# Kernel optimization log

Measured on AMD Instinct MI355X. Metric: run time of the kernel, lower is better.

Reference implementation:

```python
import jax, jax.numpy as jnp
import numpy as np

D_MODEL = 512
N_HEADS = 8
D_K = D_MODEL // N_HEADS


def setup_inputs() -> dict:
    key = jax.random.key(0)
    ks = jax.random.split(key, 12)
    B, S = 2, 4096
    std = 1.0 / np.sqrt(D_MODEL)
    inp = {
        "q": jax.random.normal(ks[0], (B, S, D_MODEL), jnp.float32),
        "k": jax.random.normal(ks[1], (B, S, D_MODEL), jnp.float32),
        "v": jax.random.normal(ks[2], (B, S, D_MODEL), jnp.float32),
        "Wq": jax.random.normal(ks[3], (D_MODEL, D_MODEL), jnp.float32) * std,
        "bq": jnp.zeros((D_MODEL,), jnp.float32),
        "Wk": jax.random.normal(ks[4], (D_MODEL, D_MODEL), jnp.float32) * std,
        "bk": jnp.zeros((D_MODEL,), jnp.float32),
        "Wv": jax.random.normal(ks[5], (D_MODEL, D_MODEL), jnp.float32) * std,
        "bv": jnp.zeros((D_MODEL,), jnp.float32),
        "Wo": jax.random.normal(ks[6], (D_MODEL, D_MODEL), jnp.float32) * std,
        "bo": jnp.zeros((D_MODEL,), jnp.float32),
        # torch init: ones
        "time_decay": jnp.ones((1, N_HEADS, 1, 1), jnp.float32) * 0.01,
        "scale": jnp.ones((1,), jnp.float32),
    }
    return inp


def reference(q, k, v, Wq, bq, Wk, bk, Wv, bv, Wo, bo, time_decay, scale):
    B, S, _ = q.shape
    # projections (torch Linear: x @ W.T + b), reshape to [B, H, S, d_k]
    def proj(x, W, b):
        y = x @ W.T + b
        return y.reshape(B, -1, N_HEADS, D_K).transpose(0, 2, 1, 3)

    qh = proj(q, Wq, bq)
    kh = proj(k, Wk, bk)
    vh = proj(v, Wv, bv)

    # scores: [B, H, Sq, Sk]
    scores = jnp.einsum("bhqd,bhkd->bhqk", qh, kh) / np.sqrt(D_K)
    scores = scores * scale
    # exponential decay over absolute key position (per-head learnable rate)
    pos = jnp.arange(S, dtype=scores.dtype)  # key positions
    decay = jnp.exp(-time_decay * jnp.abs(pos)[None, None, None, :])  # [1,H,1,Sk]
    scores = scores * decay

    attn = jax.nn.softmax(scores, axis=-1)
    context = jnp.einsum("bhqk,bhkd->bhqd", attn, vh)
    context = context.transpose(0, 2, 1, 3).reshape(B, S, D_MODEL)
    out = context @ Wo.T + bo
    return out
```

## Files before the change

### kernel.cpp

```cpp
#include <hip/hip_runtime.h>
#include <hip/hip_bf16.h>
#include <stdint.h>

typedef __attribute__((ext_vector_type(8))) __bf16 bf16x8;
typedef __attribute__((ext_vector_type(4))) float f32x4;
typedef __attribute__((ext_vector_type(16))) float f32x16;
typedef __attribute__((ext_vector_type(8))) unsigned short ushort8;
typedef __attribute__((ext_vector_type(4))) unsigned short ushort4v;
typedef __attribute__((ext_vector_type(2))) unsigned int uint2v;
typedef __attribute__((ext_vector_type(4))) unsigned int uint4v;

__device__ __forceinline__ unsigned short bfbits(float x) {
    __bf16 b = (__bf16)x;
    return __builtin_bit_cast(unsigned short, b);
}
__device__ __forceinline__ float bf2f_u(unsigned short u) {
    return __builtin_bit_cast(float, (unsigned int)u << 16);
}

__device__ __forceinline__ f32x4 mfma16(bf16x8 a, bf16x8 b, f32x4 c) {
    return __builtin_amdgcn_mfma_f32_16x16x32_bf16(a, b, c, 0, 0, 0);
}
__device__ __forceinline__ f32x16 mfma32(bf16x8 a, bf16x8 b, f32x16 c) {
    return __builtin_amdgcn_mfma_f32_32x32x16_bf16(a, b, c, 0, 0, 0);
}

__device__ __forceinline__ unsigned int cvtpk(float lo, float hi) {
    unsigned int r;
    asm("v_cvt_pk_bf16_f32 %0, %1, %2" : "=v"(r) : "v"(lo), "v"(hi));
    return r;
}

__device__ __forceinline__ float lanepull(float src, int srcl) {
    return __builtin_bit_cast(float,
        __builtin_amdgcn_ds_bpermute(srcl * 4, __builtin_bit_cast(int, src)));
}

__device__ __forceinline__ void gload16(const void* g, void* l) {
    __builtin_amdgcn_global_load_lds(
        (const __attribute__((address_space(1))) unsigned int*)g,
        (__attribute__((address_space(3))) unsigned int*)l, 16, 0, 0);
}

__device__ __forceinline__ f32x16 zero16() {
    f32x16 r;
    #pragma unroll
    for (int i = 0; i < 16; i++) r[i] = 0.f;
    return r;
}

__device__ __forceinline__ int tail_tiles(float tdh, float scale) {
    float cut = 5.3f + __logf(fmaxf(scale, 1e-20f));
    cut = fmaxf(cut, 0.f);
    tdh = fmaxf(tdh, 1e-8f);
    int kt = (int)ceilf(cut / (tdh * 64.f));
    if (kt < 1) kt = 1;
    if (kt > 64) kt = 64;
    return kt;
}

__global__ __launch_bounds__(256) void wconv(
    const float* __restrict__ Wq, const float* __restrict__ Wk,
    const float* __restrict__ Wv, const float* __restrict__ Wo,
    unsigned short* __restrict__ Wbf)
{
    const int t    = blockIdx.x * 256 + threadIdx.x;
    const int slab = t >> 15;
    const int off8 = t & 32767;
    const float* src = (slab == 0) ? Wq : (slab == 1) ? Wk : (slab == 2) ? Wv : Wo;
    float4 a = ((const float4*)(src + off8 * 8))[0];
    float4 b = ((const float4*)(src + off8 * 8))[1];
    uint4v pk = { cvtpk(a.x, a.y), cvtpk(a.z, a.w), cvtpk(b.x, b.y), cvtpk(b.z, b.w) };
    *(uint4v*)(Wbf + (size_t)slab * 262144 + off8 * 8) = pk;
}

__global__ __launch_bounds__(256) void gemm_qkv(
    const float* __restrict__ q, const float* __restrict__ k, const float* __restrict__ v,
    const unsigned short* __restrict__ Wbf,
    const float* __restrict__ bq, const float* __restrict__ bk, const float* __restrict__ bv,
    const float* __restrict__ td, const float* __restrict__ sc,
    unsigned short* __restrict__ Qh, unsigned short* __restrict__ Kh,
    unsigned short* __restrict__ Vt)
{
    __shared__ __align__(16) char ALDS[2][16384];

    const int id  = blockIdx.x;
    const int nid = (id & 7) * 96 + (id >> 3);
    const int z   = nid >> 8;
    const int rem = nid & 255;
    const int bm  = rem >> 2;
    const int bn  = rem & 3;

    const float* A0   = (z == 0) ? q  : (z == 1) ? k  : v;
    const float* bias = (z == 0) ? bq : (z == 1) ? bk : bv;

    const int tid  = threadIdx.x;
    const int lane = tid & 63;
    const int w    = tid >> 6;
    const int wm   = w >> 1, wn = w & 1;
    const int l15  = lane & 15;
    const int g    = lane >> 4;

    const int lr  = lane >> 3;
    const int lc  = ((lane & 7) * 16) ^ (lr << 4);
    const char* asrc[4];
    #pragma unroll
    for (int j = 0; j < 4; j++)
        asrc[j] = (const char*)A0 + (size_t)(bm * 128 + w * 32 + j * 8 + lr) * 2048 + lc;
    int adst[4];
    #pragma unroll
    for (int j = 0; j < 4; j++) adst[j] = w * 4096 + j * 1024;

    const unsigned short* Bp[4];
    #pragma unroll
    for (int n = 0; n < 4; n++)
        Bp[n] = Wbf + (size_t)z * 262144
              + (size_t)(bn * 128 + wn * 64 + n * 16 + l15) * 512 + g * 8;

    f32x4 acc[4][4];
    #pragma unroll
    for (int m = 0; m < 4; m++)
        #pragma unroll
        for (int n = 0; n < 4; n++)
            acc[m][n] = (f32x4){0.f, 0.f, 0.f, 0.f};

    const int arow = l15;
    const int asw  = (arow & 7) << 4;

    #pragma unroll
    for (int j = 0; j < 4; j++) gload16(asrc[j], ALDS[0] + adst[j]);
    bf16x8 BA[4], BB[4];
    #pragma unroll
    for (int n = 0; n < 4; n++) BA[n] = *(const bf16x8*)Bp[n];

#define QKV_ITER(CUR, KK, BC, BN)                                                  \
    {                                                                              \
        asm volatile("s_waitcnt vmcnt(0)" ::: "memory");                           \
        __syncthreads();                                                           \
        if ((KK) < 15) {                                                           \
            _Pragma("unroll")                                                      \
            for (int j = 0; j < 4; j++)                                            \
                gload16(asrc[j] + (size_t)((KK) + 1) * 128,                        \
                        ALDS[(CUR) ^ 1] + adst[j]);                                \
            _Pragma("unroll")                                                      \
            for (int n = 0; n < 4; n++)                                            \
                BN[n] = *(const bf16x8*)(Bp[n] + (size_t)((KK) + 1) * 32);         \
        }                                                                          \
        bf16x8 af[4];                                                              \
        _Pragma("unroll")                                                          \
        for (int m = 0; m < 4; m++) {                                              \
            const char* base = ALDS[CUR] + (wm * 64 + m * 16 + arow) * 128;        \
            f32x4 v0 = *(const f32x4*)(base + ((g * 32) ^ asw));                   \
            f32x4 v1 = *(const f32x4*)(base + (((g * 32) | 16) ^ asw));            \
            uint4v pk = { cvtpk(v0.x, v0.y), cvtpk(v0.z, v0.w),                    \
                          cvtpk(v1.x, v1.y), cvtpk(v1.z, v1.w) };                  \
            af[m] = __builtin_bit_cast(bf16x8, pk);                                \
        }                                                                          \
        __builtin_amdgcn_s_setprio(1);                                             \
        _Pragma("unroll")                                                          \
        for (int m = 0; m < 4; m++)                                                \
            _Pragma("unroll")                                                      \
            for (int n = 0; n < 4; n++)                                            \
                acc[m][n] = mfma16(af[m], BC[n], acc[m][n]);                       \
        __builtin_amdgcn_s_setprio(0);                                             \
    }

    #pragma unroll 1
    for (int t = 0; t < 8; ++t) {
        QKV_ITER(0, 2 * t, BA, BB)
        QKV_ITER(1, 2 * t + 1, BB, BA)
    }
#undef QKV_ITER

    const float coefL = sc[0] * 0.125f * 1.44269504f;

    #pragma unroll
    for (int m = 0; m < 4; m++) {
        const int grow0 = bm * 128 + wm * 64 + m * 16 + (g << 2);
        #pragma unroll
        for (int n = 0; n < 4; n++) {
            const int gcol = bn * 128 + wn * 64 + n * 16 + l15;
            const float bv2 = bias[gcol];
            f32x4 c = acc[m][n];
            const int b = grow0 >> 12, s0 = grow0 & 4095;
            const int h = gcol >> 6, dk = gcol & 63;
            if (z == 0) {
                const size_t base = ((size_t)(b * 8 + h) * 4096 + s0) * 64 + dk;
                #pragma unroll
                for (int r = 0; r < 4; r++)
                    Qh[base + (size_t)r * 64] = bfbits((c[r] + bv2) * coefL);
            } else if (z == 1) {
                const float tdh = td[h];
                const size_t base = ((size_t)(b * 8 + h) * 4096 + s0) * 64 + dk;
                #pragma unroll
                for (int r = 0; r < 4; r++)
                    Kh[base + (size_t)r * 64] = bfbits((c[r] + bv2) * __expf(-tdh * (float)(s0 + r)));
            } else {
                ushort4v pk = { bfbits(c[0] + bv2), bfbits(c[1] + bv2),
                                bfbits(c[2] + bv2), bfbits(c[3] + bv2) };
                *(ushort4v*)&Vt[((size_t)(b * 8 + h) * 64 + dk) * 4096 + s0] = pk;
            }
        }
    }
}

__global__ __launch_bounds__(256) void gemm_out(
    const unsigned short* __restrict__ Actx, const unsigned short* __restrict__ Wob,
    const float* __restrict__ bias, float* __restrict__ Out)
{
    __shared__ __align__(16) char ALDS[2][16384];

    const int id  = blockIdx.x;
    const int nid = (id & 7) * 64 + (id >> 3);
    const int bm  = nid >> 3;
    const int bn  = nid & 7;

    const int tid  = threadIdx.x;
    const int lane = tid & 63;
    const int w    = tid >> 6;
    const int wm   = w >> 1, wn = w & 1;
    const int l15  = lane & 15;
    const int g    = lane >> 4;

    const int lr  = lane >> 3;
    const int lc  = ((lane & 7) * 16) ^ (lr << 4);
    const char* asrc[4];
    #pragma unroll
    for (int j = 0; j < 4; j++)
        asrc[j] = (const char*)Actx + (size_t)(bm * 128 + w * 32 + j * 8 + lr) * 1024 + lc;
    int adst[4];
    #pragma unroll
    for (int j = 0; j < 4; j++) adst[j] = w * 4096 + j * 1024;

    const unsigned short* Bp[2];
    #pragma unroll
    for (int n = 0; n < 2; n++)
        Bp[n] = Wob + (size_t)(bn * 64 + wn * 32 + n * 16 + l15) * 512 + g * 8;

    f32x4 acc[4][2];
    #pragma unroll
    for (int m = 0; m < 4; m++)
        #pragma unroll
        for (int n = 0; n < 2; n++)
            acc[m][n] = (f32x4){0.f, 0.f, 0.f, 0.f};

    const int arow = l15;
    const int asw  = (arow & 7) << 4;

    #pragma unroll
    for (int j = 0; j < 4; j++) gload16(asrc[j], ALDS[0] + adst[j]);
    bf16x8 BA[2][2], BB[2][2];
    #pragma unroll
    for (int n = 0; n < 2; n++) {
        BA[n][0] = *(const bf16x8*)Bp[n];
        BA[n][1] = *(const bf16x8*)(Bp[n] + 32);
    }

#define OUT_ITER(CUR, KK, BC, BN)                                                  \
    {                                                                              \
        asm volatile("s_waitcnt vmcnt(0)" ::: "memory");                           \
        __syncthreads();                                                           \
        if ((KK) < 7) {                                                            \
            _Pragma("unroll")                                                      \
            for (int j = 0; j < 4; j++)                                            \
                gload16(asrc[j] + (size_t)((KK) + 1) * 128,                        \
                        ALDS[(CUR) ^ 1] + adst[j]);                                \
            _Pragma("unroll")                                                      \
            for (int n = 0; n < 2; n++) {                                          \
                BN[n][0] = *(const bf16x8*)(Bp[n] + (size_t)((KK) + 1) * 64);      \
                BN[n][1] = *(const bf16x8*)(Bp[n] + (size_t)((KK) + 1) * 64 + 32); \
            }                                                                      \
        }                                                                          \
        bf16x8 af[4][2];                                                           \
        _Pragma("unroll")                                                          \
        for (int m = 0; m < 4; m++) {                                              \
            const char* base = ALDS[CUR] + (wm * 64 + m * 16 + arow) * 128;        \
            af[m][0] = *(const bf16x8*)(base + ((g * 16) ^ asw));                  \
            af[m][1] = *(const bf16x8*)(base + ((64 + g * 16) ^ asw));             \
        }                                                                          \
        __builtin_amdgcn_s_setprio(1);                                             \
        _Pragma("unroll")                                                          \
        for (int m = 0; m < 4; m++)                                                \
            _Pragma("unroll")                                                      \
            for (int n = 0; n < 2; n++) {                                          \
                acc[m][n] = mfma16(af[m][0], BC[n][0], acc[m][n]);                 \
                acc[m][n] = mfma16(af[m][1], BC[n][1], acc[m][n]);                 \
            }                                                                      \
        __builtin_amdgcn_s_setprio(0);                                             \
    }

    #pragma unroll 1
    for (int t = 0; t < 4; ++t) {
        OUT_ITER(0, 2 * t, BA, BB)
        OUT_ITER(1, 2 * t + 1, BB, BA)
    }
#undef OUT_ITER

    #pragma unroll
    for (int m = 0; m < 4; m++) {
        const int grow0 = bm * 128 + wm * 64 + m * 16 + (g << 2);
        #pragma unroll
        for (int n = 0; n < 2; n++) {
            const int gcol = bn * 64 + wn * 32 + n * 16 + l15;
            const float bv2 = bias[gcol];
            f32x4 c = acc[m][n];
            #pragma unroll
            for (int r = 0; r < 4; r++)
                Out[(size_t)(grow0 + r) * 512 + gcol] = c[r] + bv2;
        }
    }
}

__global__ __launch_bounds__(512) void tail_pre(
    const unsigned short* __restrict__ Kh, const unsigned short* __restrict__ Vt,
    const float* __restrict__ td, const float* __restrict__ sc,
    unsigned short* __restrict__ Mt, float* __restrict__ SumV, float* __restrict__ KsL)
{
    __shared__ __align__(16) char KLDS[2][8192];
    __shared__ float redM[4][32][32];
    __shared__ float redv[64];
    __shared__ float redk[64];

    const int blk  = blockIdx.x;
    const int bh   = blk >> 1;
    const int half = blk & 1;
    const int h    = bh & 7;
    const int tid  = threadIdx.x;
    const int w    = tid >> 6;
    const int lane = tid & 63;
    const int l31  = lane & 31, hl = lane >> 5;
    const int d2q  = w & 1, d1q = (w >> 1) & 1, ksub = w >> 2;

    const int KT  = tail_tiles(td[h], sc[0]);
    const int K0  = KT * 64;
    const int nk  = 4096 - K0;
    const int kh0 = ((nk >> 1) + 63) & ~63;
    const int kcnt = half ? (nk - kh0) : kh0;
    const int kbeg = K0 + half * kh0;
    const int nch  = kcnt >> 6;

    const int lr = lane >> 3;
    const int r8 = (w * 8 + lr) & 7;
    const char* ksrc = (const char*)Kh + (size_t)(bh * 4096 + kbeg + w * 8 + lr) * 128
                     + (((lane & 7) * 16) ^ (r8 << 4));
    const int kdst = w * 1024;

    const unsigned short* Vp = Vt + (size_t)(bh * 64 + d2q * 32 + l31) * 4096 + kbeg;

    f32x16 macc = zero16();
    float sumv = 0.f, ksum = 0.f;

    if (nch > 0) gload16(ksrc, KLDS[0] + kdst);

    #pragma unroll 1
    for (int ch = 0; ch < nch; ++ch) {
        asm volatile("s_waitcnt vmcnt(0)" ::: "memory");
        __syncthreads();
        if (ch + 1 < nch)
            gload16(ksrc + (size_t)(ch + 1) * 8192, KLDS[(ch + 1) & 1] + kdst);
        const char* kb = KLDS[ch & 1];

        #pragma unroll
        for (int mf = 0; mf < 2; mf++) {
            const int kloc0 = ksub * 32 + mf * 16 + hl * 8;
            ushort8 kbv;
            #pragma unroll
            for (int e = 0; e < 8; e++) {
                const int row = kloc0 + e;
                kbv[e] = *(const unsigned short*)(kb + row * 128
                          + ((d1q * 64 + l31 * 2) ^ ((row & 7) << 4)));
            }
            if (d2q == 0) {
                #pragma unroll
                for (int e = 0; e < 8; e++) ksum += bf2f_u(kbv[e]);
            }
            bf16x8 av = *(const bf16x8*)(Vp + ch * 64 + kloc0);
            if (d1q == 0) {
                ushort8 au = __builtin_bit_cast(ushort8, av);
                #pragma unroll
                for (int e = 0; e < 8; e++) sumv += bf2f_u(au[e]);
            }
            macc = mfma32(av, __builtin_bit_cast(bf16x8, kbv), macc);
        }
    }

    sumv += __shfl_xor(sumv, 32);
    ksum += __shfl_xor(ksum, 32);

    const int quad = d2q * 2 + d1q;
    __syncthreads();
    if (ksub == 0) {
        #pragma unroll
        for (int r = 0; r < 16; r++) {
            const int row = (r & 3) + 8 * (r >> 2) + 4 * hl;
            redM[quad][row][l31] = macc[r];
        }
        if (d1q == 0 && hl == 0) redv[d2q * 32 + l31] = sumv;
        if (d2q == 0 && hl == 0) redk[d1q * 32 + l31] = ksum;
    }
    __syncthreads();
    if (ksub == 1) {
        unsigned short* Mb = Mt + (size_t)half * 16 * 4096 + (size_t)bh * 4096;
        #pragma unroll
        for (int r = 0; r < 16; r++) {
            const int row = (r & 3) + 8 * (r >> 2) + 4 * hl;
            const float mv = (macc[r] + redM[quad][row][l31]) * 0.6931472f;
            Mb[(size_t)(d2q * 32 + row) * 64 + d1q * 32 + l31] = bfbits(mv);
        }
        if (d1q == 0 && hl == 0)
            SumV[half * 1024 + bh * 64 + d2q * 32 + l31] = sumv + redv[d2q * 32 + l31];
        if (d2q == 0 && hl == 0)
            KsL[half * 1024 + bh * 64 + d1q * 32 + l31] = (ksum + redk[d1q * 32 + l31]) * 0.6931472f;
    }
}

__global__ __launch_bounds__(256, 4) void attn_decay(
    const unsigned short* __restrict__ Qh, const unsigned short* __restrict__ Kh,
    const unsigned short* __restrict__ Vt, const float* __restrict__ td,
    const float* __restrict__ sc,
    const unsigned short* __restrict__ Mt, const float* __restrict__ SumV,
    const float* __restrict__ KsL, unsigned short* __restrict__ ctx)
{
    __shared__ __align__(16) char LDSB[32768];

    const int tid  = threadIdx.x;
    const int lane = tid & 63;
    const int w    = tid >> 6;
    const int qg   = w >> 1;
    const int ws   = w & 1;
    const int l31  = lane & 31;
    const int hl   = lane >> 5;

    const int i  = blockIdx.x;
    const int bh = ((i & 7) << 1) | ((i >> 9) & 1);
    const int qt = (i >> 3) & 63;
    const int h  = bh & 7;
    const int b  = bh >> 3;

    const int KT = tail_tiles(td[h], sc[0]);
    const int nk = 4096 - KT * 64;

    bf16x8 qf[4];
    {
        const unsigned short* Qp =
            Qh + ((size_t)bh * 4096 + qt * 64 + qg * 32 + l31) * 64 + hl * 8;
        #pragma unroll
        for (int c = 0; c < 4; c++)
            qf[c] = *(const bf16x8*)(Qp + c * 16);
    }

    f32x16 o0 = zero16(), o1 = zero16();
    float lp = 0.f;

    const char* kgp0; const char* kgp1; const char* vgp0; const char* vgp1;
    int ldsoff0, ldsoff1;
    {
        const size_t kbaseB = (size_t)bh * 4096 * 64 * 2;
        const size_t vbaseB = (size_t)bh * 64 * 4096 * 2;
        const int p0 = w * 2048 + lane * 16;
        const int r0 = p0 >> 7, c0 = p0 & 127, sw0 = (r0 & 7) << 4;
        const int p1 = w * 2048 + 1024 + lane * 16;
        const int r1 = p1 >> 7, c1 = p1 & 127, sw1 = (r1 & 7) << 4;
        kgp0 = (const char*)Kh + kbaseB + (size_t)r0 * 128  + (c0 ^ sw0);
        kgp1 = (const char*)Kh + kbaseB + (size_t)r1 * 128  + (c1 ^ sw1);
        vgp0 = (const char*)Vt + vbaseB + (size_t)r0 * 8192 + (c0 ^ sw0);
        vgp1 = (const char*)Vt + vbaseB + (size_t)r1 * 8192 + (c1 ^ sw1);
        ldsoff0 = w * 2048;
        ldsoff1 = w * 2048 + 1024;
    }
    gload16(kgp0, LDSB + ldsoff0);
    gload16(kgp1, LDSB + ldsoff1);
    gload16(vgp0, LDSB + 16384 + ldsoff0);
    gload16(vgp1, LDSB + 16384 + ldsoff1);
    kgp0 += 8192; kgp1 += 8192; vgp0 += 128; vgp1 += 128;

    const int krow = ws * 32 + l31;
    const int ksw  = (krow & 7) << 4;

#define ATTN_TILE(CUR, KT_IDX)                                                    \
    {                                                                             \
        asm volatile("s_waitcnt vmcnt(0)" ::: "memory");                          \
        __syncthreads();                                                          \
        if ((KT_IDX) + 1 < KT) {                                                  \
            gload16(kgp0, LDSB + ((CUR) ^ 1) * 8192 + ldsoff0);                   \
            gload16(kgp1, LDSB + ((CUR) ^ 1) * 8192 + ldsoff1);                   \
            gload16(vgp0, LDSB + 16384 + ((CUR) ^ 1) * 8192 + ldsoff0);           \
            gload16(vgp1, LDSB + 16384 + ((CUR) ^ 1) * 8192 + ldsoff1);           \
            kgp0 += 8192; kgp1 += 8192; vgp0 += 128; vgp1 += 128;                 \
        }                                                                         \
        const char* kb = LDSB + (CUR) * 8192;                                     \
        const char* vb = LDSB + 16384 + (CUR) * 8192;                             \
        f32x16 s = zero16();                                                      \
        __builtin_amdgcn_s_setprio(1);                                            \
        _Pragma("unroll")                                                         \
        for (int c = 0; c < 4; c++) {                                             \
            bf16x8 kf = *(const bf16x8*)(kb + krow * 128 + ((c * 32 + hl * 16) ^ ksw)); \
            s = mfma32(kf, qf[c], s);                                             \
        }                                                                         \
        __builtin_amdgcn_s_setprio(0);                                            \
        float p[16];                                                              \
        _Pragma("unroll")                                                         \
        for (int r = 0; r < 16; r++) {                                            \
            p[r] = __builtin_amdgcn_exp2f(s[r]);                                  \
            lp += p[r];                                                           \
        }                                                                         \
        unsigned int W0 = cvtpk(p[0], p[1]),   W1 = cvtpk(p[2], p[3]);            \
        unsigned int W2 = cvtpk(p[4], p[5]),   W3 = cvtpk(p[6], p[7]);            \
        unsigned int W4 = cvtpk(p[8], p[9]),   W5 = cvtpk(p[10], p[11]);          \
        unsigned int W6 = cvtpk(p[12], p[13]), W7 = cvtpk(p[14], p[15]);          \
        uint2v r02 = __builtin_amdgcn_permlane32_swap(W0, W2, false, false);      \
        uint2v r13 = __builtin_amdgcn_permlane32_swap(W1, W3, false, false);      \
        uint2v r46 = __builtin_amdgcn_permlane32_swap(W4, W6, false, false);      \
        uint2v r57 = __builtin_amdgcn_permlane32_swap(W5, W7, false, false);      \
        bf16x8 pa0 = __builtin_bit_cast(bf16x8, (uint4v){r02.x, r13.x, r02.y, r13.y}); \
        bf16x8 pa1 = __builtin_bit_cast(bf16x8, (uint4v){r46.x, r57.x, r46.y, r57.y}); \
        __builtin_amdgcn_s_setprio(1);                                            \
        {                                                                         \
            const int vr0  = l31;                                                 \
            const int vsw0 = (vr0 & 7) << 4;                                      \
            bf16x8 va = *(const bf16x8*)(vb + vr0 * 128 + ((ws * 64 + hl * 16) ^ vsw0));      \
            bf16x8 vb2 = *(const bf16x8*)(vb + vr0 * 128 + ((ws * 64 + 32 + hl * 16) ^ vsw0));\
            o0 = mfma32(pa0, va, o0);                                             \
            o0 = mfma32(pa1, vb2, o0);                                            \
            const int vr1  = 32 + l31;                                            \
            const int vsw1 = (vr1 & 7) << 4;                                      \
            bf16x8 vc = *(const bf16x8*)(vb + vr1 * 128 + ((ws * 64 + hl * 16) ^ vsw1));      \
            bf16x8 vd = *(const bf16x8*)(vb + vr1 * 128 + ((ws * 64 + 32 + hl * 16) ^ vsw1)); \
            o1 = mfma32(pa0, vc, o1);                                             \
            o1 = mfma32(pa1, vd, o1);                                             \
        }                                                                         \
        __builtin_amdgcn_s_setprio(0);                                            \
    }

    const int KT2 = KT >> 1;
    #pragma unroll 1
    for (int t = 0; t < KT2; ++t) {
        ATTN_TILE(0, 2 * t)
        ATTN_TILE(1, 2 * t + 1)
    }
    if (KT & 1) {
        ATTN_TILE(0, KT - 1)
    }
#undef ATTN_TILE

    if (ws == 0 && nk > 0) {
        float qk = 0.f;
        #pragma unroll
        for (int c = 0; c < 4; c++) {
            ushort8 qb = __builtin_bit_cast(ushort8, qf[c]);
            #pragma unroll
            for (int e = 0; e < 8; e++) {
                const int idx = c * 16 + hl * 8 + e;
                qk += bf2f_u(qb[e]) * (KsL[bh * 64 + idx] + KsL[1024 + bh * 64 + idx]);
            }
        }
        qk += __shfl_xor(qk, 32);
        if (hl == 0) lp += (float)nk + qk;

        #pragma unroll
        for (int half = 0; half < 2; half++) {
            const unsigned short* Mb = Mt + (size_t)half * 16 * 4096 + (size_t)bh * 4096;
            #pragma unroll
            for (int c = 0; c < 4; c++) {
                bf16x8 m0 = *(const bf16x8*)(Mb + (size_t)l31 * 64 + c * 16 + hl * 8);
                bf16x8 m1 = *(const bf16x8*)(Mb + (size_t)(32 + l31) * 64 + c * 16 + hl * 8);
                o0 = mfma32(qf[c], m0, o0);
                o1 = mfma32(qf[c], m1, o1);
            }
        }
        const float sv0 = SumV[bh * 64 + l31]      + SumV[1024 + bh * 64 + l31];
        const float sv1 = SumV[bh * 64 + 32 + l31] + SumV[1024 + bh * 64 + 32 + l31];
        #pragma unroll
        for (int r = 0; r < 16; r++) { o0[r] += sv0; o1[r] += sv1; }
    }

    float lw = lp + __shfl_xor(lp, 32);
    __syncthreads();
    float* lscr = (float*)(LDSB + 16384);
    if (lane < 32)
        lscr[(qg * 2 + ws) * 32 + lane] = lw;
    __syncthreads();
    const float pl2 = lscr[(qg * 2 + (ws ^ 1)) * 32 + l31];
    const float myscale = 1.f / (lw + pl2);
    #pragma unroll
    for (int rc = 0; rc < 4; rc++)
        #pragma unroll
        for (int j = 0; j < 4; j++) {
            const float a = lanepull(myscale, rc * 8 + hl * 4 + j);
            o0[rc * 4 + j] *= a;
            o1[rc * 4 + j] *= a;
        }
    __syncthreads();
    float* Oscr = (float*)(LDSB + qg * 8192);
    if (ws == 1) {
        #pragma unroll
        for (int reg = 0; reg < 16; reg++) {
            const int row = (reg & 3) + 8 * (reg >> 2) + 4 * hl;
            Oscr[row * 64 + l31]      = o0[reg];
            Oscr[row * 64 + 32 + l31] = o1[reg];
        }
    }
    __syncthreads();
    if (ws == 0) {
        #pragma unroll
        for (int reg = 0; reg < 16; reg++) {
            const int row = (reg & 3) + 8 * (reg >> 2) + 4 * hl;
            const float v0 = o0[reg] + Oscr[row * 64 + l31];
            const float v1 = o1[reg] + Oscr[row * 64 + 32 + l31];
            const int srow_ = qt * 64 + qg * 32 + row;
            const size_t idx = ((size_t)b * 4096 + srow_) * 512 + h * 64;
            ctx[idx + l31]      = bfbits(v0);
            ctx[idx + 32 + l31] = bfbits(v1);
        }
    }
}

extern "C" void kernel_launch(void* const* d_in, const int* in_sizes, int n_in,
                              void* d_out, int out_size, void* d_ws, size_t ws_size,
                              hipStream_t stream)
{
    (void)in_sizes; (void)n_in; (void)out_size; (void)ws_size;
    const float* q  = (const float*)d_in[0];
    const float* k  = (const float*)d_in[1];
    const float* v  = (const float*)d_in[2];
    const float* Wq = (const float*)d_in[3];
    const float* bq = (const float*)d_in[4];
    const float* Wk = (const float*)d_in[5];
    const float* bk = (const float*)d_in[6];
    const float* Wv = (const float*)d_in[7];
    const float* bv = (const float*)d_in[8];
    const float* Wo = (const float*)d_in[9];
    const float* bo = (const float*)d_in[10];
    const float* td = (const float*)d_in[11];
    const float* sc = (const float*)d_in[12];

    unsigned short* Qh  = (unsigned short*)d_ws;
    unsigned short* Kh  = Qh + (size_t)16 * 4096 * 64;
    unsigned short* Vt  = Kh + (size_t)16 * 4096 * 64;
    unsigned short* ctx = Vt + (size_t)16 * 4096 * 64;
    unsigned short* Wbf = ctx + (size_t)16 * 4096 * 64;

    unsigned short* Mt   = (unsigned short*)d_out;
    float*          SumV = (float*)((char*)d_out + 2 * 16 * 4096 * 2);
    float*          KsL  = SumV + 2 * 1024;

    wconv<<<dim3(512), 256, 0, stream>>>(Wq, Wk, Wv, Wo, Wbf);
    gemm_qkv<<<dim3(768), 256, 0, stream>>>(q, k, v, Wbf, bq, bk, bv, td, sc, Qh, Kh, Vt);
    tail_pre<<<dim3(32), 512, 0, stream>>>(Kh, Vt, td, sc, Mt, SumV, KsL);
    attn_decay<<<dim3(1024), 256, 0, stream>>>(Qh, Kh, Vt, td, sc, Mt, SumV, KsL, ctx);
    gemm_out<<<dim3(512), 256, 0, stream>>>(ctx, Wbf + (size_t)3 * 262144, bo, (float*)d_out);
}
```

Baseline: 122.5 us.

## Make GEMM warps own private A rows with triple-buffered LDS, drop block barriers

Both projection GEMMs now have each warp load and consume only its own 32 rows of A, so the per-iteration __syncthreads is removed and replaced by a per-warp vmcnt wait. A per-warp triple-buffered LDS ring prefetches two K-steps ahead, and the K loop is fully unrolled. The warp tile changes from 64x64 (or 64x32) to 32x128 (or 32x64), so each warp now loads the full B column set itself, which doubles B global/L2 loads per block and uses more registers. LDS use grows from 32 KB to 48 KB per block, which may lower occupancy.

```diff
diff --git a/kernel.cpp b/kernel.cpp
--- a/kernel.cpp
+++ b/kernel.cpp
@@ -82,7 +82,7 @@
     unsigned short* __restrict__ Qh, unsigned short* __restrict__ Kh,
     unsigned short* __restrict__ Vt)
 {
-    __shared__ __align__(16) char ALDS[2][16384];
+    __shared__ __align__(16) char ALDS[49152];
 
     const int id  = blockIdx.x;
     const int nid = (id & 7) * 96 + (id >> 3);
@@ -97,89 +97,92 @@
     const int tid  = threadIdx.x;
     const int lane = tid & 63;
     const int w    = tid >> 6;
-    const int wm   = w >> 1, wn = w & 1;
     const int l15  = lane & 15;
     const int g    = lane >> 4;
 
-    const int lr  = lane >> 3;
-    const int lc  = ((lane & 7) * 16) ^ (lr << 4);
+    const int lr = lane >> 3;
+    const int lc = ((lane & 7) * 16) ^ (lr << 4);
     const char* asrc[4];
     #pragma unroll
     for (int j = 0; j < 4; j++)
         asrc[j] = (const char*)A0 + (size_t)(bm * 128 + w * 32 + j * 8 + lr) * 2048 + lc;
-    int adst[4];
-    #pragma unroll
-    for (int j = 0; j < 4; j++) adst[j] = w * 4096 + j * 1024;
-
-    const unsigned short* Bp[4];
-    #pragma unroll
-    for (int n = 0; n < 4; n++)
+    char* const wlds = ALDS + w * 12288;
+
+    const unsigned short* Bp[8];
+    #pragma unroll
+    for (int n = 0; n < 8; n++)
         Bp[n] = Wbf + (size_t)z * 262144
-              + (size_t)(bn * 128 + wn * 64 + n * 16 + l15) * 512 + g * 8;
-
-    f32x4 acc[4][4];
-    #pragma unroll
-    for (int m = 0; m < 4; m++)
-        #pragma unroll
-        for (int n = 0; n < 4; n++)
+              + (size_t)(bn * 128 + n * 16 + l15) * 512 + g * 8;
+
+    f32x4 acc[2][8];
+    #pragma unroll
+    for (int m = 0; m < 2; m++)
+        #pragma unroll
+        for (int n = 0; n < 8; n++)
             acc[m][n] = (f32x4){0.f, 0.f, 0.f, 0.f};
 
-    const int arow = l15;
-    const int asw  = (arow & 7) << 4;
-
-    #pragma unroll
-    for (int j = 0; j < 4; j++) gload16(asrc[j], ALDS[0] + adst[j]);
-    bf16x8 BA[4], BB[4];
-    #pragma unroll
-    for (int n = 0; n < 4; n++) BA[n] = *(const bf16x8*)Bp[n];
-
-#define QKV_ITER(CUR, KK, BC, BN)                                                  \
+    const int asw = (l15 & 7) << 4;
+    const int c0  = (g * 32) ^ asw;
+
+    #pragma unroll
+    for (int j = 0; j < 4; j++) gload16(asrc[j], wlds + j * 1024);
+    bf16x8 BA[8], BB[8];
+    #pragma unroll
+    for (int n = 0; n < 8; n++) BA[n] = *(const bf16x8*)Bp[n];
+    #pragma unroll
+    for (int j = 0; j < 4; j++) gload16(asrc[j] + 128, wlds + 4096 + j * 1024);
+
+#define QKV_ITER(KK, BC, BN)                                                       \
     {                                                                              \
-        asm volatile("s_waitcnt vmcnt(0)" ::: "memory");                           \
-        __syncthreads();                                                           \
-        if ((KK) < 15) {                                                           \
-            _Pragma("unroll")                                                      \
-            for (int j = 0; j < 4; j++)                                            \
-                gload16(asrc[j] + (size_t)((KK) + 1) * 128,                        \
-                        ALDS[(CUR) ^ 1] + adst[j]);                                \
-            _Pragma("unroll")                                                      \
-            for (int n = 0; n < 4; n++)                                            \
-                BN[n] = *(const bf16x8*)(Bp[n] + (size_t)((KK) + 1) * 32);         \
-        }                                                                          \
-        bf16x8 af[4];                                                              \
+        asm volatile("s_waitcnt vmcnt(4)" ::: "memory");                           \
+        bf16x8 af[2];                                                              \
         _Pragma("unroll")                                                          \
-        for (int m = 0; m < 4; m++) {                                              \
-            const char* base = ALDS[CUR] + (wm * 64 + m * 16 + arow) * 128;        \
-            f32x4 v0 = *(const f32x4*)(base + ((g * 32) ^ asw));                   \
-            f32x4 v1 = *(const f32x4*)(base + (((g * 32) | 16) ^ asw));            \
+        for (int m = 0; m < 2; m++) {                                              \
+            const char* base = wlds + ((KK) % 3) * 4096 + (m * 16 + l15) * 128;    \
+            f32x4 v0 = *(const f32x4*)(base + c0);                                 \
+            f32x4 v1 = *(const f32x4*)(base + (c0 ^ 16));                          \
             uint4v pk = { cvtpk(v0.x, v0.y), cvtpk(v0.z, v0.w),                    \
                           cvtpk(v1.x, v1.y), cvtpk(v1.z, v1.w) };                  \
             af[m] = __builtin_bit_cast(bf16x8, pk);                                \
         }                                                                          \
+        if ((KK) + 1 < 16) {                                                       \
+            _Pragma("unroll")                                                      \
+            for (int n = 0; n < 8; n++)                                            \
+                BN[n] = *(const bf16x8*)(Bp[n] + ((KK) + 1) * 32);                 \
+        }                                                                          \
+        if ((KK) + 2 < 16) {                                                       \
+            _Pragma("unroll")                                                      \
+            for (int j = 0; j < 4; j++)                                            \
+                gload16(asrc[j] + (size_t)((KK) + 2) * 128,                        \
+                        wlds + (((KK) + 2) % 3) * 4096 + j * 1024);                \
+        }                                                                          \
         __builtin_amdgcn_s_setprio(1);                                             \
         _Pragma("unroll")                                                          \
-        for (int m = 0; m < 4; m++)                                                \
+        for (int m = 0; m < 2; m++)                                                \
             _Pragma("unroll")                                                      \
-            for (int n = 0; n < 4; n++)                                            \
+            for (int n = 0; n < 8; n++)                                            \
                 acc[m][n] = mfma16(af[m], BC[n], acc[m][n]);                       \
         __builtin_amdgcn_s_setprio(0);                                             \
     }
 
-    #pragma unroll 1
-    for (int t = 0; t < 8; ++t) {
-        QKV_ITER(0, 2 * t, BA, BB)
-        QKV_ITER(1, 2 * t + 1, BB, BA)
-    }
+    QKV_ITER(0,  BA, BB)  QKV_ITER(1,  BB, BA)
+    QKV_ITER(2,  BA, BB)  QKV_ITER(3,  BB, BA)
+    QKV_ITER(4,  BA, BB)  QKV_ITER(5,  BB, BA)
+    QKV_ITER(6,  BA, BB)  QKV_ITER(7,  BB, BA)
+    QKV_ITER(8,  BA, BB)  QKV_ITER(9,  BB, BA)
+    QKV_ITER(10, BA, BB)  QKV_ITER(11, BB, BA)
+    QKV_ITER(12, BA, BB)  QKV_ITER(13, BB, BA)
+    QKV_ITER(14, BA, BB)  QKV_ITER(15, BB, BA)
 #undef QKV_ITER
 
     const float coefL = sc[0] * 0.125f * 1.44269504f;
 
     #pragma unroll
-    for (int m = 0; m < 4; m++) {
-        const int grow0 = bm * 128 + wm * 64 + m * 16 + (g << 2);
-        #pragma unroll
-        for (int n = 0; n < 4; n++) {
-            const int gcol = bn * 128 + wn * 64 + n * 16 + l15;
+    for (int m = 0; m < 2; m++) {
+        const int grow0 = bm * 128 + w * 32 + m * 16 + (g << 2);
+        #pragma unroll
+        for (int n = 0; n < 8; n++) {
+            const int gcol = bn * 128 + n * 16 + l15;
             const float bv2 = bias[gcol];
             f32x4 c = acc[m][n];
             const int b = grow0 >> 12, s0 = grow0 & 4095;
@@ -208,7 +211,7 @@
     const unsigned short* __restrict__ Actx, const unsigned short* __restrict__ Wob,
     const float* __restrict__ bias, float* __restrict__ Out)
 {
-    __shared__ __align__(16) char ALDS[2][16384];
+    __shared__ __align__(16) char ALDS[49152];
 
     const int id  = blockIdx.x;
     const int nid = (id & 7) * 64 + (id >> 3);
@@ -218,90 +221,89 @@
     const int tid  = threadIdx.x;
     const int lane = tid & 63;
     const int w    = tid >> 6;
-    const int wm   = w >> 1, wn = w & 1;
     const int l15  = lane & 15;
     const int g    = lane >> 4;
 
-    const int lr  = lane >> 3;
-    const int lc  = ((lane & 7) * 16) ^ (lr << 4);
+    const int lr = lane >> 3;
+    const int lc = ((lane & 7) * 16) ^ (lr << 4);
     const char* asrc[4];
     #pragma unroll
     for (int j = 0; j < 4; j++)
         asrc[j] = (const char*)Actx + (size_t)(bm * 128 + w * 32 + j * 8 + lr) * 1024 + lc;
-    int adst[4];
-    #pragma unroll
-    for (int j = 0; j < 4; j++) adst[j] = w * 4096 + j * 1024;
-
-    const unsigned short* Bp[2];
-    #pragma unroll
-    for (int n = 0; n < 2; n++)
-        Bp[n] = Wob + (size_t)(bn * 64 + wn * 32 + n * 16 + l15) * 512 + g * 8;
-
-    f32x4 acc[4][2];
-    #pragma unroll
-    for (int m = 0; m < 4; m++)
-        #pragma unroll
-        for (int n = 0; n < 2; n++)
+    char* const wlds = ALDS + w * 12288;
+
+    const unsigned short* Bp[4];
+    #pragma unroll
+    for (int n = 0; n < 4; n++)
+        Bp[n] = Wob + (size_t)(bn * 64 + n * 16 + l15) * 512 + g * 8;
+
+    f32x4 acc[2][4];
+    #pragma unroll
+    for (int m = 0; m < 2; m++)
+        #pragma unroll
+        for (int n = 0; n < 4; n++)
             acc[m][n] = (f32x4){0.f, 0.f, 0.f, 0.f};
 
-    const int arow = l15;
-    const int asw  = (arow & 7) << 4;
-
-    #pragma unroll
-    for (int j = 0; j < 4; j++) gload16(asrc[j], ALDS[0] + adst[j]);
-    bf16x8 BA[2][2], BB[2][2];
-    #pragma unroll
-    for (int n = 0; n < 2; n++) {
+    const int asw = (l15 & 7) << 4;
+    const int c0  = (g * 16) ^ asw;
+
+    #pragma unroll
+    for (int j = 0; j < 4; j++) gload16(asrc[j], wlds + j * 1024);
+    bf16x8 BA[4][2], BB[4][2];
+    #pragma unroll
+    for (int n = 0; n < 4; n++) {
         BA[n][0] = *(const bf16x8*)Bp[n];
         BA[n][1] = *(const bf16x8*)(Bp[n] + 32);
     }
-
-#define OUT_ITER(CUR, KK, BC, BN)                                                  \
+    #pragma unroll
+    for (int j = 0; j < 4; j++) gload16(asrc[j] + 128, wlds + 4096 + j * 1024);
+
+#define OUT_ITER(KK, BC, BN)                                                       \
     {                                                                              \
-        asm volatile("s_waitcnt vmcnt(0)" ::: "memory");                           \
-        __syncthreads();                                                           \
-        if ((KK) < 7) {                                                            \
+        asm volatile("s_waitcnt vmcnt(4)" ::: "memory");                           \
+        bf16x8 af[2][2];                                                           \
+        _Pragma("unroll")                                                          \
+        for (int m = 0; m < 2; m++) {                                              \
+            const char* base = wlds + ((KK) % 3) * 4096 + (m * 16 + l15) * 128;    \
+            af[m][0] = *(const bf16x8*)(base + c0);                                \
+            af[m][1] = *(const bf16x8*)(base + ((64 + g * 16) ^ asw));             \
+        }                                                                          \
+        if ((KK) + 1 < 8) {                                                        \
+            _Pragma("unroll")                                                      \
+            for (int n = 0; n < 4; n++) {                                          \
+                BN[n][0] = *(const bf16x8*)(Bp[n] + ((KK) + 1) * 64);              \
+                BN[n][1] = *(const bf16x8*)(Bp[n] + ((KK) + 1) * 64 + 32);         \
+            }                                                                      \
+        }                                                                          \
+        if ((KK) + 2 < 8) {                                                        \
             _Pragma("unroll")                                                      \
             for (int j = 0; j < 4; j++)                                            \
-                gload16(asrc[j] + (size_t)((KK) + 1) * 128,                        \
-                        ALDS[(CUR) ^ 1] + adst[j]);                                \
-            _Pragma("unroll")                                                      \
-            for (int n = 0; n < 2; n++) {                                          \
-                BN[n][0] = *(const bf16x8*)(Bp[n] + (size_t)((KK) + 1) * 64);      \
-                BN[n][1] = *(const bf16x8*)(Bp[n] + (size_t)((KK) + 1) * 64 + 32); \
-            }                                                                      \
-        }                                                                          \
-        bf16x8 af[4][2];                                                           \
-        _Pragma("unroll")                                                          \
-        for (int m = 0; m < 4; m++) {                                              \
-            const char* base = ALDS[CUR] + (wm * 64 + m * 16 + arow) * 128;        \
-            af[m][0] = *(const bf16x8*)(base + ((g * 16) ^ asw));                  \
-            af[m][1] = *(const bf16x8*)(base + ((64 + g * 16) ^ asw));             \
+                gload16(asrc[j] + (size_t)((KK) + 2) * 128,                        \
+                        wlds + (((KK) + 2) % 3) * 4096 + j * 1024);                \
         }                                                                          \
         __builtin_amdgcn_s_setprio(1);                                             \
         _Pragma("unroll")                                                          \
-        for (int m = 0; m < 4; m++)                                                \
+        for (int m = 0; m < 2; m++)                                                \
             _Pragma("unroll")                                                      \
-            for (int n = 0; n < 2; n++) {                                          \
+            for (int n = 0; n < 4; n++) {                                          \
                 acc[m][n] = mfma16(af[m][0], BC[n][0], acc[m][n]);                 \
                 acc[m][n] = mfma16(af[m][1], BC[n][1], acc[m][n]);                 \
             }                                                                      \
         __builtin_amdgcn_s_setprio(0);                                             \
     }
 
-    #pragma unroll 1
-    for (int t = 0; t < 4; ++t) {
-        OUT_ITER(0, 2 * t, BA, BB)
-        OUT_ITER(1, 2 * t + 1, BB, BA)
-    }
+    OUT_ITER(0, BA, BB)  OUT_ITER(1, BB, BA)
+    OUT_ITER(2, BA, BB)  OUT_ITER(3, BB, BA)
+    OUT_ITER(4, BA, BB)  OUT_ITER(5, BB, BA)
+    OUT_ITER(6, BA, BB)  OUT_ITER(7, BB, BA)
 #undef OUT_ITER
 
     #pragma unroll
-    for (int m = 0; m < 4; m++) {
-        const int grow0 = bm * 128 + wm * 64 + m * 16 + (g << 2);
-        #pragma unroll
-        for (int n = 0; n < 2; n++) {
-            const int gcol = bn * 64 + wn * 32 + n * 16 + l15;
+    for (int m = 0; m < 2; m++) {
+        const int grow0 = bm * 128 + w * 32 + m * 16 + (g << 2);
+        #pragma unroll
+        for (int n = 0; n < 4; n++) {
+            const int gcol = bn * 64 + n * 16 + l15;
             const float bv2 = bias[gcol];
             f32x4 c = acc[m][n];
             #pragma unroll
```

Measured after the change: 138.0 us. +12.6%, slower.
